# Performance work log

Hardware: AMD Instinct MI355X
Metric: run time of the kernel (lower is better)

## Reference

```python
import jax, jax.numpy as jnp
import numpy as np

N_NODES = 50000
N_EDGES = 800000
N_GRAPHS = 512
HIDDEN = 256
NODE_FEAT = 9
LAYERS = 4


def setup_inputs() -> dict:
    key = jax.random.key(0)
    ks = jax.random.split(key, 9)
    x = jax.random.normal(ks[0], (N_NODES, NODE_FEAT), dtype=jnp.float32)
    edge_index = jax.random.randint(ks[1], (2, N_EDGES), 0, N_NODES, dtype=jnp.int64)
    batch = jnp.sort(jax.random.randint(ks[2], (N_NODES,), 0, N_GRAPHS, dtype=jnp.int64))
    embed_W = jax.random.normal(ks[3], (NODE_FEAT, HIDDEN), dtype=jnp.float32) * (1.0 / np.sqrt(NODE_FEAT))
    embed_b = jnp.zeros((HIDDEN,), dtype=jnp.float32)
    conv_W = jax.random.normal(ks[4], (LAYERS, HIDDEN, HIDDEN), dtype=jnp.float32) * (1.0 / np.sqrt(HIDDEN))
    conv_b = jnp.zeros((LAYERS, HIDDEN), dtype=jnp.float32)
    out_W = jax.random.normal(ks[5], (HIDDEN, 1), dtype=jnp.float32) * (1.0 / np.sqrt(HIDDEN))
    out_b = jnp.zeros((1,), dtype=jnp.float32)
    return {"x": x, "edge_index": edge_index, "batch": batch,
            "embed_W": embed_W, "embed_b": embed_b,
            "conv_W": conv_W, "conv_b": conv_b,
            "out_W": out_W, "out_b": out_b}


def reference(x, edge_index, batch, embed_W, embed_b, conv_W, conv_b, out_W, out_b):
    n = x.shape[0]
    src, dst = edge_index[0], edge_index[1]
    # GCN symmetric normalization with self-loops: deg includes the self-loop (+1)
    deg = jax.ops.segment_sum(jnp.ones(src.shape[0], x.dtype), dst, num_segments=n) + 1.0
    dinv = jax.lax.rsqrt(deg)                       # [N]
    norm_e = dinv[src] * dinv[dst]                  # [E] edge coefficient
    self_coef = (dinv * dinv)[:, None]              # [N,1] self-loop coefficient

    h = jax.nn.relu(x @ embed_W + embed_b)          # [N,H]
    for l in range(conv_W.shape[0]):
        hw = h @ conv_W[l]                          # [N,H] transform first
        msg = hw[src] * norm_e[:, None]             # [E,H] gather + scale
        agg = jax.ops.segment_sum(msg, dst, num_segments=n)  # scatter-add
        agg = agg + hw * self_coef                  # self-loop contribution
        h = jax.nn.relu(agg + conv_b[l])

    # global mean pool over graph ids
    sums = jax.ops.segment_sum(h, batch, num_segments=N_GRAPHS)           # [G,H]
    cnt = jax.ops.segment_sum(jnp.ones(n, h.dtype), batch, num_segments=N_GRAPHS)
    pooled = sums / jnp.maximum(cnt, 1.0)[:, None]
    return pooled @ out_W + out_b                   # [G,1]
```

## Files before the change

kernel.cpp:

```cpp
#include <hip/hip_runtime.h>

#define N_NODES 50000
#define N_EDGES 800000
#define N_GRAPHS 512
#define HIDDEN 256
#define NODE_FEAT 9
#define LAYERS 4
#define BUCKET 64

typedef float floatx4 __attribute__((ext_vector_type(4)));
typedef short short8 __attribute__((ext_vector_type(8)));

__device__ __forceinline__ float bf2f(unsigned u) {
    unsigned v = u << 16;
    float f;
    __builtin_memcpy(&f, &v, 4);
    return f;
}
__device__ __forceinline__ unsigned short f2bf(float f) {
    unsigned v;
    __builtin_memcpy(&v, &f, 4);
    v += 0x7FFFu + ((v >> 16) & 1u);
    return (unsigned short)(v >> 16);
}

__global__ void fillb_kernel(const int* __restrict__ src, const int* __restrict__ dst,
                             int* __restrict__ cnt, int* __restrict__ col_src, int E) {
    int e = blockIdx.x * blockDim.x + threadIdx.x;
    if (e < E) {
        int d = dst[e];
        int pos = atomicAdd(&cnt[d], 1);
        if (pos < BUCKET) col_src[d * BUCKET + pos] = src[e];
    }
}

__global__ void dinv_kernel(const int* __restrict__ cnt, float* __restrict__ dinv, int N) {
    int i = blockIdx.x * blockDim.x + threadIdx.x;
    if (i < N) dinv[i] = rsqrtf((float)(cnt[i] + 1));
}

__global__ void findstart_kernel(const int* __restrict__ batch, int* __restrict__ gstart) {
    int g = blockIdx.x * blockDim.x + threadIdx.x;
    if (g > N_GRAPHS) return;
    if (g == N_GRAPHS) { gstart[g] = N_NODES; return; }
    int lo = 0, hi = N_NODES;
    while (lo < hi) {
        int mid = (lo + hi) >> 1;
        if (batch[mid] < g) lo = mid + 1; else hi = mid;
    }
    gstart[g] = lo;
}

__global__ __launch_bounds__(256) void packW_kernel(const float* __restrict__ W,
                                                    unsigned short* __restrict__ Wsw) {
    int idx = blockIdx.x * 256 + threadIdx.x;
    int lane = idx & 63;
    int ct   = (idx >> 6) & 15;
    int ks   = (idx >> 10) & 7;
    int l    = idx >> 13;
    int n = ct * 16 + (lane & 15);
    int kbase = ks * 32 + (lane >> 4) * 8;
    const float* Wl = W + (size_t)l * HIDDEN * HIDDEN;
    alignas(16) unsigned short tmp[8];
    #pragma unroll
    for (int j = 0; j < 8; j++)
        tmp[j] = f2bf(Wl[(size_t)(kbase + j) * HIDDEN + n]);
    *(uint4*)&Wsw[(size_t)idx * 8] = *(const uint4*)tmp;
}

__global__ __launch_bounds__(256) void embed_kernel(const float* __restrict__ x,
                                                    const float* __restrict__ W,
                                                    const float* __restrict__ b,
                                                    unsigned short* __restrict__ h) {
    int n = blockIdx.x;
    int c = threadIdx.x;
    float acc = b[c];
    #pragma unroll
    for (int k = 0; k < NODE_FEAT; k++)
        acc += x[n * NODE_FEAT + k] * W[k * HIDDEN + c];
    h[(size_t)n * HIDDEN + c] = f2bf(fmaxf(acc, 0.0f));
}

__global__ __launch_bounds__(256, 2) void gemm_mfma(const unsigned short* __restrict__ hin,
                                                    const unsigned short* __restrict__ Wsw,
                                                    unsigned short* __restrict__ hwout, int N) {
    __shared__ unsigned short As[64][264];
    int t = threadIdx.x;
    int wv = t >> 6, lane = t & 63, quad = lane >> 4, l15 = lane & 15;
    int n0 = blockIdx.x * 64;
    const uint4* h4 = (const uint4*)hin;

    uint4 av[8];
    #pragma unroll
    for (int i = 0; i < 8; i++) {
        int j = t + i * 256;
        int r = j >> 5;
        int c = j & 31;
        int n = n0 + r;
        av[i] = make_uint4(0u, 0u, 0u, 0u);
        if (n < N) av[i] = h4[(size_t)n * 32 + c];
    }
    const short8* Wl = (const short8*)Wsw;
    short8 bq[3][4];
    #pragma unroll
    for (int p = 0; p < 2; p++)
        #pragma unroll
        for (int ci = 0; ci < 4; ci++)
            bq[p][ci] = Wl[(size_t)(p * 16 + wv * 4 + ci) * 64 + lane];
    #pragma unroll
    for (int i = 0; i < 8; i++) {
        int j = t + i * 256;
        int r = j >> 5;
        int c = j & 31;
        *(uint4*)&As[r][c * 8] = av[i];
    }
    __syncthreads();

    floatx4 acc[4][4];
    #pragma unroll
    for (int i = 0; i < 4; i++)
        #pragma unroll
        for (int j = 0; j < 4; j++)
            acc[i][j] = (floatx4){0.f, 0.f, 0.f, 0.f};

    #pragma unroll
    for (int ks = 0; ks < 8; ks++) {
        if (ks < 6) {
            #pragma unroll
            for (int ci = 0; ci < 4; ci++)
                bq[(ks + 2) % 3][ci] = Wl[(size_t)((ks + 2) * 16 + wv * 4 + ci) * 64 + lane];
        }
        short8 a[4];
        #pragma unroll
        for (int rt = 0; rt < 4; rt++)
            a[rt] = *(const short8*)&As[rt * 16 + l15][ks * 32 + quad * 8];
        #pragma unroll
        for (int rt = 0; rt < 4; rt++)
            #pragma unroll
            for (int ci = 0; ci < 4; ci++)
                acc[rt][ci] = __builtin_amdgcn_mfma_f32_16x16x32_bf16(a[rt], bq[ks % 3][ci], acc[rt][ci], 0, 0, 0);
    }

    __syncthreads();
    #pragma unroll
    for (int rt = 0; rt < 4; rt++) {
        #pragma unroll
        for (int ci = 0; ci < 4; ci++) {
            int col = (wv * 4 + ci) * 16 + l15;
            int rowb = rt * 16 + quad * 4;
            #pragma unroll
            for (int reg = 0; reg < 4; reg++)
                As[rowb + reg][col] = f2bf(acc[rt][ci][reg]);
        }
    }
    __syncthreads();
    #pragma unroll
    for (int i = 0; i < 8; i++) {
        int j = t + i * 256;
        int r = j >> 5;
        int c = j & 31;
        int n = n0 + r;
        if (n < N)
            *(uint4*)&hwout[(size_t)n * HIDDEN + c * 8] = *(const uint4*)&As[r][c * 8];
    }
}

__global__ __launch_bounds__(256) void agg_kernel(const unsigned short* __restrict__ hw,
                                                  const int* __restrict__ cnt,
                                                  const int* __restrict__ col_src,
                                                  const float* __restrict__ dinv,
                                                  const float* __restrict__ bias,
                                                  unsigned short* __restrict__ hout) {
    __shared__ uint2 sEdge[4][64];
    int wv = threadIdx.x >> 6, lane = threadIdx.x & 63;
    int n = blockIdx.x * 4 + wv;
    if (n >= N_NODES) return;
    float dn = dinv[n];
    int deg = cnt[n]; if (deg > BUCKET) deg = BUCKET;

    uint2 s2 = ((const uint2*)(hw + (size_t)n * HIDDEN))[lane];
    float4 b4 = *(const float4*)&bias[4 * lane];
    float selfc = dn * dn;
    float a0 = bf2f(s2.x & 0xFFFFu) * selfc + b4.x;
    float a1 = bf2f(s2.x >> 16)     * selfc + b4.y;
    float a2 = bf2f(s2.y & 0xFFFFu) * selfc + b4.z;
    float a3 = bf2f(s2.y >> 16)     * selfc + b4.w;

    if (lane < deg) {
        int s = col_src[n * BUCKET + lane];
        float nr = dinv[s] * dn;
        unsigned nrb;
        __builtin_memcpy(&nrb, &nr, 4);
        sEdge[wv][lane] = make_uint2((unsigned)s, nrb);
    }
    for (int i = 0; i < deg; i++) {
        uint2 p = sEdge[wv][i];
        float nr;
        __builtin_memcpy(&nr, &p.y, 4);
        uint2 u = ((const uint2*)(hw + (size_t)p.x * HIDDEN))[lane];
        a0 += nr * bf2f(u.x & 0xFFFFu);
        a1 += nr * bf2f(u.x >> 16);
        a2 += nr * bf2f(u.y & 0xFFFFu);
        a3 += nr * bf2f(u.y >> 16);
    }
    unsigned p0 = (unsigned)f2bf(fmaxf(a0, 0.0f)) | ((unsigned)f2bf(fmaxf(a1, 0.0f)) << 16);
    unsigned p1 = (unsigned)f2bf(fmaxf(a2, 0.0f)) | ((unsigned)f2bf(fmaxf(a3, 0.0f)) << 16);
    ((uint2*)(hout + (size_t)n * HIDDEN))[lane] = make_uint2(p0, p1);
}

__global__ __launch_bounds__(256) void pool2_kernel(const unsigned short* __restrict__ h,
                                                    const int* __restrict__ gstart,
                                                    const float* __restrict__ outW,
                                                    const float* __restrict__ outb,
                                                    float* __restrict__ out) {
    __shared__ float sred[4];
    int g = blockIdx.x;
    int t = threadIdx.x;
    int s = gstart[g], e = gstart[g + 1];
    int half = t >> 7;
    int tc = t & 127;
    float w0 = outW[2 * tc], w1 = outW[2 * tc + 1];
    float acc = 0.0f;
    for (int n = s + half; n < e; n += 2) {
        unsigned u = *(const unsigned*)&h[(size_t)n * HIDDEN + 2 * tc];
        acc += w0 * bf2f(u & 0xFFFFu) + w1 * bf2f(u >> 16);
    }
    #pragma unroll
    for (int off = 32; off > 0; off >>= 1) acc += __shfl_down(acc, off, 64);
    if ((t & 63) == 0) sred[t >> 6] = acc;
    __syncthreads();
    if (t == 0) {
        float tot = sred[0] + sred[1] + sred[2] + sred[3];
        float cntf = (float)(e - s);
        out[g] = tot / fmaxf(cntf, 1.0f) + outb[0];
    }
}

extern "C" void kernel_launch(void* const* d_in, const int* in_sizes, int n_in,
                              void* d_out, int out_size, void* d_ws, size_t ws_size,
                              hipStream_t stream) {
    const float* x     = (const float*)d_in[0];
    const int*   edge  = (const int*)d_in[1];
    const int*   src   = edge;
    const int*   dst   = edge + N_EDGES;
    const int*   batch = (const int*)d_in[2];
    const float* embW  = (const float*)d_in[3];
    const float* embb  = (const float*)d_in[4];
    const float* convW = (const float*)d_in[5];
    const float* convb = (const float*)d_in[6];
    const float* outW  = (const float*)d_in[7];
    const float* outb  = (const float*)d_in[8];
    float* out = (float*)d_out;

    char* ws = (char*)d_ws;
    size_t off = 0;
    auto take = [&](size_t bytes) { char* p = ws + off; off += (bytes + 255) & ~(size_t)255; return p; };
    int*   cnt     = (int*)  take((size_t)N_NODES * 4);
    int*   col_src = (int*)  take((size_t)N_NODES * BUCKET * 4);
    float* dinv    = (float*)take((size_t)N_NODES * 4);
    int*   gstart  = (int*)  take((size_t)(N_GRAPHS + 1) * 4);
    unsigned short* Wsw = (unsigned short*)take((size_t)LAYERS * 8 * 16 * 64 * 8 * 2);
    unsigned short* h0  = (unsigned short*)take((size_t)N_NODES * HIDDEN * 2);
    unsigned short* h1  = (unsigned short*)take((size_t)N_NODES * HIDDEN * 2);

    hipMemsetAsync(cnt, 0, (size_t)N_NODES * 4, stream);

    fillb_kernel<<<(N_EDGES + 255) / 256, 256, 0, stream>>>(src, dst, cnt, col_src, N_EDGES);
    dinv_kernel<<<(N_NODES + 255) / 256, 256, 0, stream>>>(cnt, dinv, N_NODES);
    findstart_kernel<<<3, 256, 0, stream>>>(batch, gstart);

    packW_kernel<<<128, 256, 0, stream>>>(convW, Wsw);
    embed_kernel<<<N_NODES, 256, 0, stream>>>(x, embW, embb, h0);

    unsigned short* ha = h0;
    unsigned short* hb = h1;
    for (int l = 0; l < LAYERS; l++) {
        gemm_mfma<<<(N_NODES + 63) / 64, 256, 0, stream>>>(ha, Wsw + (size_t)l * 65536, hb, N_NODES);
        agg_kernel<<<(N_NODES + 3) / 4, 256, 0, stream>>>(hb, cnt, col_src, dinv, convb + (size_t)l * HIDDEN, ha);
    }

    pool2_kernel<<<N_GRAPHS, 256, 0, stream>>>(ha, gstart, outW, outb, out);
}
```

Baseline: 459.7 us.

## Fuse embed into first GEMM, fold pooling into last aggregation, precompute edge norms

The embedding is fused into the first layer GEMM, which now has each wave compute a full 16x256 output tile, reading A directly from global memory with no shared-memory staging. The final aggregation computes the per-node dot product with the output weights so that pooling only reduces scalars. Edge normalisation coefficients are precomputed once into an (src, coef) array so the aggregation kernels skip the dinv gathers, and the small setup kernels are merged. This removes the embed kernel, the write and reread of the last hidden layer, and redundant per-layer gathers, at the cost of an extra 25MB esrc buffer and a GEMM with no A-tile reuse across waves.

Result: slower. 497.1 us (+8.2%).

```diff
diff --git a/kernel.cpp b/kernel.cpp
--- a/kernel.cpp
+++ b/kernel.cpp
@@ -7,9 +7,11 @@
 #define NODE_FEAT 9
 #define LAYERS 4
 #define BUCKET 64
+#define NTILE (N_NODES / 16)
 
 typedef float floatx4 __attribute__((ext_vector_type(4)));
 typedef short short8 __attribute__((ext_vector_type(8)));
+typedef unsigned uint2v __attribute__((ext_vector_type(2)));
 
 __device__ __forceinline__ float bf2f(unsigned u) {
     unsigned v = u << 16;
@@ -34,21 +36,37 @@
     }
 }
 
-__global__ void dinv_kernel(const int* __restrict__ cnt, float* __restrict__ dinv, int N) {
-    int i = blockIdx.x * blockDim.x + threadIdx.x;
-    if (i < N) dinv[i] = rsqrtf((float)(cnt[i] + 1));
-}
-
-__global__ void findstart_kernel(const int* __restrict__ batch, int* __restrict__ gstart) {
-    int g = blockIdx.x * blockDim.x + threadIdx.x;
-    if (g > N_GRAPHS) return;
-    if (g == N_GRAPHS) { gstart[g] = N_NODES; return; }
-    int lo = 0, hi = N_NODES;
-    while (lo < hi) {
-        int mid = (lo + hi) >> 1;
-        if (batch[mid] < g) lo = mid + 1; else hi = mid;
-    }
-    gstart[g] = lo;
+__global__ __launch_bounds__(256) void aux_kernel(const int* __restrict__ cnt,
+                                                  float* __restrict__ dinv,
+                                                  const int* __restrict__ batch,
+                                                  int* __restrict__ gstart) {
+    int i = blockIdx.x * 256 + threadIdx.x;
+    if (i < N_NODES) dinv[i] = rsqrtf((float)(cnt[i] + 1));
+    int g = i - N_NODES;
+    if (g >= 0 && g <= N_GRAPHS) {
+        if (g == N_GRAPHS) { gstart[g] = N_NODES; return; }
+        int lo = 0, hi = N_NODES;
+        while (lo < hi) {
+            int mid = (lo + hi) >> 1;
+            if (batch[mid] < g) lo = mid + 1; else hi = mid;
+        }
+        gstart[g] = lo;
+    }
+}
+
+__global__ __launch_bounds__(256) void eprep_kernel(const int* __restrict__ cnt,
+                                                    const int* __restrict__ col_src,
+                                                    const float* __restrict__ dinv,
+                                                    uint2* __restrict__ esrc) {
+    int i = blockIdx.x * 256 + threadIdx.x;
+    int n = i >> 6, e = i & 63;
+    int deg = cnt[n]; if (deg > BUCKET) deg = BUCKET;
+    if (e < deg) {
+        int s = col_src[i];
+        float nr = dinv[s] * dinv[n];
+        unsigned nrb; __builtin_memcpy(&nrb, &nr, 4);
+        esrc[i] = make_uint2((unsigned)s, nrb);
+    }
 }
 
 __global__ __launch_bounds__(256) void packW_kernel(const float* __restrict__ W,
@@ -68,106 +86,121 @@
     *(uint4*)&Wsw[(size_t)idx * 8] = *(const uint4*)tmp;
 }
 
-__global__ __launch_bounds__(256) void embed_kernel(const float* __restrict__ x,
-                                                    const float* __restrict__ W,
-                                                    const float* __restrict__ b,
-                                                    unsigned short* __restrict__ h) {
-    int n = blockIdx.x;
-    int c = threadIdx.x;
-    float acc = b[c];
-    #pragma unroll
-    for (int k = 0; k < NODE_FEAT; k++)
-        acc += x[n * NODE_FEAT + k] * W[k * HIDDEN + c];
-    h[(size_t)n * HIDDEN + c] = f2bf(fmaxf(acc, 0.0f));
-}
-
-__global__ __launch_bounds__(256, 2) void gemm_mfma(const unsigned short* __restrict__ hin,
-                                                    const unsigned short* __restrict__ Wsw,
-                                                    unsigned short* __restrict__ hwout, int N) {
-    __shared__ unsigned short As[64][264];
+__global__ __launch_bounds__(256) void gemm_mfma(const unsigned short* __restrict__ hin,
+                                                 const unsigned short* __restrict__ Wsw,
+                                                 unsigned short* __restrict__ hwout) {
+    __shared__ unsigned short sC[4][16][264];
     int t = threadIdx.x;
     int wv = t >> 6, lane = t & 63, quad = lane >> 4, l15 = lane & 15;
-    int n0 = blockIdx.x * 64;
-    const uint4* h4 = (const uint4*)hin;
-
-    uint4 av[8];
+    int tile = blockIdx.x * 4 + wv;
+    if (tile >= NTILE) return;
+    int r0 = tile * 16;
+    const short8* Arow = (const short8*)(hin + (size_t)(r0 + l15) * HIDDEN);
+    const short8* Wl = (const short8*)Wsw;
+
+    floatx4 acc[16];
+    #pragma unroll
+    for (int ci = 0; ci < 16; ci++) acc[ci] = (floatx4){0.f, 0.f, 0.f, 0.f};
+
+    #pragma unroll
+    for (int ks = 0; ks < 8; ks++) {
+        short8 a = Arow[ks * 4 + quad];
+        short8 bq[16];
+        #pragma unroll
+        for (int ci = 0; ci < 16; ci++)
+            bq[ci] = Wl[(size_t)(ks * 16 + ci) * 64 + lane];
+        #pragma unroll
+        for (int ci = 0; ci < 16; ci++)
+            acc[ci] = __builtin_amdgcn_mfma_f32_16x16x32_bf16(a, bq[ci], acc[ci], 0, 0, 0);
+    }
+
+    #pragma unroll
+    for (int ci = 0; ci < 16; ci++)
+        #pragma unroll
+        for (int reg = 0; reg < 4; reg++)
+            sC[wv][quad * 4 + reg][ci * 16 + l15] = f2bf(acc[ci][reg]);
     #pragma unroll
     for (int i = 0; i < 8; i++) {
-        int j = t + i * 256;
-        int r = j >> 5;
-        int c = j & 31;
-        int n = n0 + r;
-        av[i] = make_uint4(0u, 0u, 0u, 0u);
-        if (n < N) av[i] = h4[(size_t)n * 32 + c];
-    }
+        int row = i * 2 + (lane >> 5);
+        int c8  = lane & 31;
+        *(uint4*)&hwout[(size_t)(r0 + row) * HIDDEN + c8 * 8] = *(const uint4*)&sC[wv][row][c8 * 8];
+    }
+}
+
+__global__ __launch_bounds__(256) void embed_gemm(const float* __restrict__ x,
+                                                  const float* __restrict__ embW,
+                                                  const float* __restrict__ embb,
+                                                  const unsigned short* __restrict__ Wsw,
+                                                  unsigned short* __restrict__ hwout) {
+    __shared__ unsigned short sC[4][16][264];
+    int t = threadIdx.x;
+    int wv = t >> 6, lane = t & 63, quad = lane >> 4, l15 = lane & 15;
+    int tile = blockIdx.x * 4 + wv;
+    if (tile >= NTILE) return;
+    int r0 = tile * 16;
+    int row = r0 + l15;
+
+    float xr[NODE_FEAT];
+    #pragma unroll
+    for (int k = 0; k < NODE_FEAT; k++) xr[k] = x[(size_t)row * NODE_FEAT + k];
+
+    short8 af[8];
+    #pragma unroll
+    for (int ks = 0; ks < 8; ks++) {
+        int c0 = ks * 32 + quad * 8;
+        float4 a0 = *(const float4*)&embb[c0];
+        float4 a1 = *(const float4*)&embb[c0 + 4];
+        #pragma unroll
+        for (int k = 0; k < NODE_FEAT; k++) {
+            float4 w0 = *(const float4*)&embW[k * HIDDEN + c0];
+            float4 w1 = *(const float4*)&embW[k * HIDDEN + c0 + 4];
+            a0.x += xr[k] * w0.x; a0.y += xr[k] * w0.y;
+            a0.z += xr[k] * w0.z; a0.w += xr[k] * w0.w;
+            a1.x += xr[k] * w1.x; a1.y += xr[k] * w1.y;
+            a1.z += xr[k] * w1.z; a1.w += xr[k] * w1.w;
+        }
+        af[ks][0] = (short)f2bf(fmaxf(a0.x, 0.f));
+        af[ks][1] = (short)f2bf(fmaxf(a0.y, 0.f));
+        af[ks][2] = (short)f2bf(fmaxf(a0.z, 0.f));
+        af[ks][3] = (short)f2bf(fmaxf(a0.w, 0.f));
+        af[ks][4] = (short)f2bf(fmaxf(a1.x, 0.f));
+        af[ks][5] = (short)f2bf(fmaxf(a1.y, 0.f));
+        af[ks][6] = (short)f2bf(fmaxf(a1.z, 0.f));
+        af[ks][7] = (short)f2bf(fmaxf(a1.w, 0.f));
+    }
+
     const short8* Wl = (const short8*)Wsw;
-    short8 bq[3][4];
-    #pragma unroll
-    for (int p = 0; p < 2; p++)
-        #pragma unroll
-        for (int ci = 0; ci < 4; ci++)
-            bq[p][ci] = Wl[(size_t)(p * 16 + wv * 4 + ci) * 64 + lane];
+    floatx4 acc[16];
+    #pragma unroll
+    for (int ci = 0; ci < 16; ci++) acc[ci] = (floatx4){0.f, 0.f, 0.f, 0.f};
+
+    #pragma unroll
+    for (int ks = 0; ks < 8; ks++) {
+        short8 bq[16];
+        #pragma unroll
+        for (int ci = 0; ci < 16; ci++)
+            bq[ci] = Wl[(size_t)(ks * 16 + ci) * 64 + lane];
+        #pragma unroll
+        for (int ci = 0; ci < 16; ci++)
+            acc[ci] = __builtin_amdgcn_mfma_f32_16x16x32_bf16(af[ks], bq[ci], acc[ci], 0, 0, 0);
+    }
+
+    #pragma unroll
+    for (int ci = 0; ci < 16; ci++)
+        #pragma unroll
+        for (int reg = 0; reg < 4; reg++)
+            sC[wv][quad * 4 + reg][ci * 16 + l15] = f2bf(acc[ci][reg]);
     #pragma unroll
     for (int i = 0; i < 8; i++) {
-        int j = t + i * 256;
-        int r = j >> 5;
-        int c = j & 31;
-        *(uint4*)&As[r][c * 8] = av[i];
-    }
-    __syncthreads();
-
-    floatx4 acc[4][4];
-    #pragma unroll
-    for (int i = 0; i < 4; i++)
-        #pragma unroll
-        for (int j = 0; j < 4; j++)
-            acc[i][j] = (floatx4){0.f, 0.f, 0.f, 0.f};
-
-    #pragma unroll
-    for (int ks = 0; ks < 8; ks++) {
-        if (ks < 6) {
-            #pragma unroll
-            for (int ci = 0; ci < 4; ci++)
-                bq[(ks + 2) % 3][ci] = Wl[(size_t)((ks + 2) * 16 + wv * 4 + ci) * 64 + lane];
-        }
-        short8 a[4];
-        #pragma unroll
-        for (int rt = 0; rt < 4; rt++)
-            a[rt] = *(const short8*)&As[rt * 16 + l15][ks * 32 + quad * 8];
-        #pragma unroll
-        for (int rt = 0; rt < 4; rt++)
-            #pragma unroll
-            for (int ci = 0; ci < 4; ci++)
-                acc[rt][ci] = __builtin_amdgcn_mfma_f32_16x16x32_bf16(a[rt], bq[ks % 3][ci], acc[rt][ci], 0, 0, 0);
-    }
-
-    __syncthreads();
-    #pragma unroll
-    for (int rt = 0; rt < 4; rt++) {
-        #pragma unroll
-        for (int ci = 0; ci < 4; ci++) {
-            int col = (wv * 4 + ci) * 16 + l15;
-            int rowb = rt * 16 + quad * 4;
-            #pragma unroll
-            for (int reg = 0; reg < 4; reg++)
-                As[rowb + reg][col] = f2bf(acc[rt][ci][reg]);
-        }
-    }
-    __syncthreads();
-    #pragma unroll
-    for (int i = 0; i < 8; i++) {
-        int j = t + i * 256;
-        int r = j >> 5;
-        int c = j & 31;
-        int n = n0 + r;
-        if (n < N)
-            *(uint4*)&hwout[(size_t)n * HIDDEN + c * 8] = *(const uint4*)&As[r][c * 8];
+        int r = i * 2 + (lane >> 5);
+        int c8 = lane & 31;
+        *(uint4*)&hwout[(size_t)(r0 + r) * HIDDEN + c8 * 8] = *(const uint4*)&sC[wv][r][c8 * 8];
     }
 }
 
 __global__ __launch_bounds__(256) void agg_kernel(const unsigned short* __restrict__ hw,
                                                   const int* __restrict__ cnt,
-                                                  const int* __restrict__ col_src,
+                                                  const uint2* __restrict__ esrc,
                                                   const float* __restrict__ dinv,
                                                   const float* __restrict__ bias,
                                                   unsigned short* __restrict__ hout) {
@@ -186,13 +219,7 @@
     float a2 = bf2f(s2.y & 0xFFFFu) * selfc + b4.z;
     float a3 = bf2f(s2.y >> 16)     * selfc + b4.w;
 
-    if (lane < deg) {
-        int s = col_src[n * BUCKET + lane];
-        float nr = dinv[s] * dn;
-        unsigned nrb;
-        __builtin_memcpy(&nrb, &nr, 4);
-        sEdge[wv][lane] = make_uint2((unsigned)s, nrb);
-    }
+    if (lane < deg) sEdge[wv][lane] = esrc[n * BUCKET + lane];
     for (int i = 0; i < deg; i++) {
         uint2 p = sEdge[wv][i];
         float nr;
@@ -208,32 +235,59 @@
     ((uint2*)(hout + (size_t)n * HIDDEN))[lane] = make_uint2(p0, p1);
 }
 
-__global__ __launch_bounds__(256) void pool2_kernel(const unsigned short* __restrict__ h,
-                                                    const int* __restrict__ gstart,
-                                                    const float* __restrict__ outW,
-                                                    const float* __restrict__ outb,
-                                                    float* __restrict__ out) {
-    __shared__ float sred[4];
+__global__ __launch_bounds__(256) void agg_dot_kernel(const unsigned short* __restrict__ hw,
+                                                      const int* __restrict__ cnt,
+                                                      const uint2* __restrict__ esrc,
+                                                      const float* __restrict__ dinv,
+                                                      const float* __restrict__ bias,
+                                                      const float* __restrict__ outW,
+                                                      float* __restrict__ dotv) {
+    __shared__ uint2 sEdge[4][64];
+    int wv = threadIdx.x >> 6, lane = threadIdx.x & 63;
+    int n = blockIdx.x * 4 + wv;
+    if (n >= N_NODES) return;
+    float dn = dinv[n];
+    int deg = cnt[n]; if (deg > BUCKET) deg = BUCKET;
+
+    uint2 s2 = ((const uint2*)(hw + (size_t)n * HIDDEN))[lane];
+    float4 b4 = *(const float4*)&bias[4 * lane];
+    float selfc = dn * dn;
+    float a0 = bf2f(s2.x & 0xFFFFu) * selfc + b4.x;
+    float a1 = bf2f(s2.x >> 16)     * selfc + b4.y;
+    float a2 = bf2f(s2.y & 0xFFFFu) * selfc + b4.z;
+    float a3 = bf2f(s2.y >> 16)     * selfc + b4.w;
+
+    if (lane < deg) sEdge[wv][lane] = esrc[n * BUCKET + lane];
+    for (int i = 0; i < deg; i++) {
+        uint2 p = sEdge[wv][i];
+        float nr;
+        __builtin_memcpy(&nr, &p.y, 4);
+        uint2 u = ((const uint2*)(hw + (size_t)p.x * HIDDEN))[lane];
+        a0 += nr * bf2f(u.x & 0xFFFFu);
+        a1 += nr * bf2f(u.x >> 16);
+        a2 += nr * bf2f(u.y & 0xFFFFu);
+        a3 += nr * bf2f(u.y >> 16);
+    }
+    float4 w = *(const float4*)&outW[4 * lane];
+    float dot = fmaxf(a0, 0.0f) * w.x + fmaxf(a1, 0.0f) * w.y
+              + fmaxf(a2, 0.0f) * w.z + fmaxf(a3, 0.0f) * w.w;
+    #pragma unroll
+    for (int off = 32; off > 0; off >>= 1) dot += __shfl_xor(dot, off, 64);
+    if (lane == 0) dotv[n] = dot;
+}
+
+__global__ __launch_bounds__(64) void finalize_kernel(const float* __restrict__ dotv,
+                                                      const int* __restrict__ gstart,
+                                                      const float* __restrict__ outb,
+                                                      float* __restrict__ out) {
     int g = blockIdx.x;
-    int t = threadIdx.x;
+    int lane = threadIdx.x;
     int s = gstart[g], e = gstart[g + 1];
-    int half = t >> 7;
-    int tc = t & 127;
-    float w0 = outW[2 * tc], w1 = outW[2 * tc + 1];
     float acc = 0.0f;
-    for (int n = s + half; n < e; n += 2) {
-        unsigned u = *(const unsigned*)&h[(size_t)n * HIDDEN + 2 * tc];
-        acc += w0 * bf2f(u & 0xFFFFu) + w1 * bf2f(u >> 16);
-    }
-    #pragma unroll
-    for (int off = 32; off > 0; off >>= 1) acc += __shfl_down(acc, off, 64);
-    if ((t & 63) == 0) sred[t >> 6] = acc;
-    __syncthreads();
-    if (t == 0) {
-        float tot = sred[0] + sred[1] + sred[2] + sred[3];
-        float cntf = (float)(e - s);
-        out[g] = tot / fmaxf(cntf, 1.0f) + outb[0];
-    }
+    for (int n = s + lane; n < e; n += 64) acc += dotv[n];
+    #pragma unroll
+    for (int off = 32; off > 0; off >>= 1) acc += __shfl_xor(acc, off, 64);
+    if (lane == 0) out[g] = acc / fmaxf((float)(e - s), 1.0f) + outb[0];
 }
 
 extern "C" void kernel_launch(void* const* d_in, const int* in_sizes, int n_in,
@@ -257,27 +311,32 @@
     auto take = [&](size_t bytes) { char* p = ws + off; off += (bytes + 255) & ~(size_t)255; return p; };
     int*   cnt     = (int*)  take((size_t)N_NODES * 4);
     int*   col_src = (int*)  take((size_t)N_NODES * BUCKET * 4);
+    uint2* esrc    = (uint2*)take((size_t)N_NODES * BUCKET * 8);
     float* dinv    = (float*)take((size_t)N_NODES * 4);
     int*   gstart  = (int*)  take((size_t)(N_GRAPHS + 1) * 4);
+    float* dotv    = (float*)take((size_t)N_NODES * 4);
     unsigned short* Wsw = (unsigned short*)take((size_t)LAYERS * 8 * 16 * 64 * 8 * 2);
     unsigned short* h0  = (unsigned short*)take((size_t)N_NODES * HIDDEN * 2);
     unsigned short* h1  = (unsigned short*)take((size_t)N_NODES * HIDDEN * 2);
 
     hipMemsetAsync(cnt, 0, (size_t)N_NODES * 4, stream);
 
+    packW_kernel<<<128, 256, 0, stream>>>(convW, Wsw);
     fillb_kernel<<<(N_EDGES + 255) / 256, 256, 0, stream>>>(src, dst, cnt, col_src, N_EDGES);
-    dinv_kernel<<<(N_NODES + 255) / 256, 256, 0, stream>>>(cnt, dinv, N_NODES);
-    findstart_kernel<<<3, 256, 0, stream>>>(batch, gstart);
-
-    packW_kernel<<<128, 256, 0, stream>>>(convW, Wsw);
-    embed_kernel<<<N_NODES, 256, 0, stream>>>(x, embW, embb, h0);
-
-    unsigned short* ha = h0;
-    unsigned short* hb = h1;
-    for (int l = 0; l < LAYERS; l++) {
-        gemm_mfma<<<(N_NODES + 63) / 64, 256, 0, stream>>>(ha, Wsw + (size_t)l * 65536, hb, N_NODES);
-        agg_kernel<<<(N_NODES + 3) / 4, 256, 0, stream>>>(hb, cnt, col_src, dinv, convb + (size_t)l * HIDDEN, ha);
-    }
-
-    pool2_kernel<<<N_GRAPHS, 256, 0, stream>>>(ha, gstart, outW, outb, out);
-}
+    aux_kernel<<<(N_NODES + N_GRAPHS + 1 + 255) / 256, 256, 0, stream>>>(cnt, dinv, batch, gstart);
+    eprep_kernel<<<(N_NODES * BUCKET) / 256, 256, 0, stream>>>(cnt, col_src, dinv, esrc);
+
+    int gblk = (NTILE + 3) / 4;
+    int ablk = (N_NODES + 3) / 4;
+
+    embed_gemm<<<gblk, 256, 0, stream>>>(x, embW, embb, Wsw, h1);
+    agg_kernel<<<ablk, 256, 0, stream>>>(h1, cnt, esrc, dinv, convb + 0 * HIDDEN, h0);
+    gemm_mfma<<<gblk, 256, 0, stream>>>(h0, Wsw + (size_t)1 * 65536, h1);
+    agg_kernel<<<ablk, 256, 0, stream>>>(h1, cnt, esrc, dinv, convb + 1 * HIDDEN, h0);
+    gemm_mfma<<<gblk, 256, 0, stream>>>(h0, Wsw + (size_t)2 * 65536, h1);
+    agg_kernel<<<ablk, 256, 0, stream>>>(h1, cnt, esrc, dinv, convb + 2 * HIDDEN, h0);
+    gemm_mfma<<<gblk, 256, 0, stream>>>(h0, Wsw + (size_t)3 * 65536, h1);
+    agg_dot_kernel<<<ablk, 256, 0, stream>>>(h1, cnt, esrc, dinv, convb + 3 * HIDDEN, outW, dotv);
+
+    finalize_kernel<<<N_GRAPHS, 64, 0, stream>>>(dotv, gstart, outb, out);
+}
```
